# Performance work log

Hardware: AMD Instinct MI355X
Metric: run time of the kernel (lower is better)

The kernel has to match this reference:

```python
import jax, jax.numpy as jnp
import numpy as np

N = 50000   # nodes
E = 800000  # edges (avg degree 16)
H = 3       # attention heads
D_IN, D_HID, D_OUT = 256, 64, 10


def setup_inputs() -> dict:
    key = jax.random.key(0)
    ks = jax.random.split(key, 8)
    x = jax.random.normal(ks[0], (N, D_IN), dtype=jnp.float32)
    edge_index = jax.random.randint(ks[1], (2, E), 0, N, dtype=jnp.int64)
    W1 = jax.random.normal(ks[2], (H, D_IN, D_HID), dtype=jnp.float32) / np.sqrt(D_IN)
    a_src1 = jax.random.normal(ks[3], (H, D_HID), dtype=jnp.float32) / np.sqrt(D_HID)
    a_dst1 = jax.random.normal(ks[4], (H, D_HID), dtype=jnp.float32) / np.sqrt(D_HID)
    W2 = jax.random.normal(ks[5], (H, D_HID, D_OUT), dtype=jnp.float32) / np.sqrt(D_HID)
    a_src2 = jax.random.normal(ks[6], (H, D_OUT), dtype=jnp.float32) / np.sqrt(D_OUT)
    a_dst2 = jax.random.normal(ks[7], (H, D_OUT), dtype=jnp.float32) / np.sqrt(D_OUT)
    return {"x": x, "edge_index": edge_index, "W1": W1, "a_src1": a_src1,
            "a_dst1": a_dst1, "W2": W2, "a_src2": a_src2, "a_dst2": a_dst2}


def gat_layer(x, src, dst, W, a_s, a_d, n):
    # x: [N, Din]; W: [H, Din, Dout]; returns [N, Dout] (heads averaged)
    z = jnp.einsum('nd,hde->nhe', x, W)                     # [N, H, Dout]
    e_src = jnp.einsum('nhe,he->nh', z, a_s)[src]           # [E, H]
    e_dst = jnp.einsum('nhe,he->nh', z, a_d)[dst]           # [E, H]
    e = jax.nn.leaky_relu(e_src + e_dst, 0.2)               # [E, H]
    # numerically-stable softmax over incoming edges of each dst node
    m = jax.lax.stop_gradient(jax.ops.segment_max(e, dst, num_segments=n))
    ex = jnp.exp(e - m[dst])                                # [E, H]
    denom = jax.ops.segment_sum(ex, dst, num_segments=n)    # [N, H]
    alpha = ex / (denom[dst] + 1e-16)                       # [E, H]
    out = jax.ops.segment_sum(z[src] * alpha[:, :, None], dst, num_segments=n)
    return out.mean(axis=1)                                 # [N, Dout]


def reference(x, edge_index, W1, a_src1, a_dst1, W2, a_src2, a_dst2):
    n = x.shape[0]
    src, dst = edge_index[0], edge_index[1]
    # dropout layers are identity in eval/deterministic mode
    h = gat_layer(x, src, dst, W1, a_src1, a_dst1, n)
    h = jax.nn.elu(h)
    h = gat_layer(h, src, dst, W2, a_src2, a_dst2, n)
    return h, jax.nn.log_softmax(h, axis=1)
```

## Files before the change

### kernel.cpp

```cpp
#include <hip/hip_runtime.h>
#include <math.h>

#define DIN  256
#define DHID 64
#define NH   3
#define DOUT 10
#define CAP  64

typedef __attribute__((ext_vector_type(8))) short bf16x8;
typedef __attribute__((ext_vector_type(4))) float f32x4;

__device__ inline unsigned short f2bf(float f) {
    unsigned u = __builtin_bit_cast(unsigned, f);
    unsigned r = (u + 0x7FFFu + ((u >> 16) & 1u)) >> 16;
    return (unsigned short)r;
}
__device__ inline float bf2f(unsigned short s) {
    unsigned u = ((unsigned)s) << 16;
    return __builtin_bit_cast(float, u);
}
__device__ inline f32x4 cvt4(ushort4 z) {
    f32x4 r;
    r[0] = bf2f(z.x); r[1] = bf2f(z.y); r[2] = bf2f(z.z); r[3] = bf2f(z.w);
    return r;
}


__global__ __launch_bounds__(256) void repack_zero_kernel(const float* __restrict__ W1,
                                                          unsigned short* __restrict__ W1p,
                                                          int* __restrict__ cursor, int N) {
    int bid = blockIdx.x;
    int tid = threadIdx.x;
    if (bid < 192) {
        int idx = bid * 256 + tid;
        int j = idx & 7, l = (idx >> 3) & 63, q = (idx >> 9) & 7, t = idx >> 12;
        int c = t * 16 + (l & 15);
        int k = q * 32 + (l >> 4) * 8 + j;
        int h = c >> 6, jj = c & 63;
        W1p[idx] = f2bf(W1[h * 16384 + k * 64 + jj]);
    } else {
        int i = (bid - 192) * 256 + tid;
        if (i < N) cursor[i] = 0;
    }
}


__global__ __launch_bounds__(256) void scatter_kernel(const int* __restrict__ src,
                                                      const int* __restrict__ dst,
                                                      int* __restrict__ cursor,
                                                      unsigned short* __restrict__ esrcp, int E) {
    int i = blockIdx.x * 256 + threadIdx.x;
    if (i < E) {
        int d = dst[i];
        int s = src[i];
        int pos = atomicAdd(cursor + d, 1);
        if (pos < CAP) esrcp[d * CAP + pos] = (unsigned short)s;
    }
}


__global__ __launch_bounds__(128) void gemm1_mfma_kernel(const float* __restrict__ x,
                                                         const bf16x8* __restrict__ W1p,
                                                         const float* __restrict__ a_s,
                                                         const float* __restrict__ a_d,
                                                         unsigned short* __restrict__ z1bf,
                                                         float* __restrict__ s1,
                                                         float* __restrict__ d1, int n) {
    __shared__ unsigned short Xs[32][272];
    int tid = threadIdx.x;
    int w = tid >> 6, lane = tid & 63;
    int m = lane & 15, quad = lane >> 4;
    int n0 = blockIdx.x * 32;

    for (int i = tid; i < 2048; i += 128) {
        int r = i >> 6, c4 = i & 63;
        int nn = n0 + r;
        float4 a = (nn < n) ? *(const float4*)(x + (size_t)nn * 256 + c4 * 4)
                            : (float4){0.f, 0.f, 0.f, 0.f};
        ushort4 b;
        b.x = f2bf(a.x); b.y = f2bf(a.y); b.z = f2bf(a.z); b.w = f2bf(a.w);
        *(ushort4*)(&Xs[r][c4 * 4]) = b;
    }
    __syncthreads();

    int rloc = w * 16 + m;
    f32x4 acc[12];
    #pragma unroll
    for (int t = 0; t < 12; ++t) acc[t] = (f32x4){0.f, 0.f, 0.f, 0.f};
    #pragma unroll
    for (int q = 0; q < 8; ++q) {
        bf16x8 af = *(const bf16x8*)(&Xs[rloc][q * 32 + quad * 8]);
        #pragma unroll
        for (int t = 0; t < 12; ++t) {
            bf16x8 bfr = W1p[(t * 8 + q) * 64 + lane];
            acc[t] = __builtin_amdgcn_mfma_f32_16x16x32_bf16(af, bfr, acc[t], 0, 0, 0);
        }
    }
    __syncthreads();

    float as_r[12], ad_r[12];
    #pragma unroll
    for (int t = 0; t < 12; ++t) { as_r[t] = a_s[t * 16 + m]; ad_r[t] = a_d[t * 16 + m]; }

    #pragma unroll
    for (int reg = 0; reg < 4; ++reg) {
        int row_loc = w * 16 + quad * 4 + reg;
        int row_out = n0 + row_loc;
        bool ok = row_out < n;
        float ps[3] = {0.f, 0.f, 0.f}, pd[3] = {0.f, 0.f, 0.f};
        #pragma unroll
        for (int t = 0; t < 12; ++t) {
            float v = acc[t][reg];
            Xs[row_loc][t * 16 + m] = f2bf(v);
            ps[t >> 2] += v * as_r[t];
            pd[t >> 2] += v * ad_r[t];
        }
        #pragma unroll
        for (int h = 0; h < 3; ++h) {
            float s = ps[h], d = pd[h];
            #pragma unroll
            for (int msk = 1; msk < 16; msk <<= 1) {
                s += __shfl_xor(s, msk, 16);
                d += __shfl_xor(d, msk, 16);
            }
            if (ok && m == 0) { s1[row_out * 4 + h] = s; d1[row_out * 4 + h] = d; }
        }
    }
    __syncthreads();

    for (int i = tid; i < 1536; i += 128) {
        int r = i / 48, c4 = i % 48;
        int nn = n0 + r;
        if (nn < n)
            *(ushort4*)(z1bf + (size_t)nn * 192 + c4 * 4) = *(const ushort4*)(&Xs[r][c4 * 4]);
    }
}


__global__ __launch_bounds__(256) void agg1_gemm2_kernel(
        const int* __restrict__ cnts, const unsigned short* __restrict__ esrcp,
        const float* __restrict__ s1, const float* __restrict__ d1,
        const unsigned short* __restrict__ z1bf,
        const float* __restrict__ W2, const float* __restrict__ as2,
        const float* __restrict__ ad2,
        unsigned short* __restrict__ z2bf,
        float* __restrict__ s2, float* __restrict__ d2, int n) {
    __shared__ float Ws[64][32];
    __shared__ float wlds[4][196];
    __shared__ float hb[4][64];
    __shared__ float tb[4][64];
    int tid = threadIdx.x;
    int lane = tid & 63, wave = tid >> 6;

    for (int idx = tid; idx < 2048; idx += 256) {
        int kk = idx >> 5, c = idx & 31;
        float wv = 0.f;
        if (c < 30) {
            int h = c / 10, j = c % 10;
            wv = W2[(h * 64 + kk) * 10 + j];
        }
        Ws[kk][c] = wv;
    }
    __syncthreads();

    int v = blockIdx.x * 4 + wave;
    if (v >= n) return;
    int cnt = cnts[v]; if (cnt > CAP) cnt = CAP;
    int m16 = lane & 15;
    int grp = lane >> 4;
    int head = grp > 2 ? 2 : grp;
    bool rowact = lane < 48;
    float dv0 = d1[v * 4], dv1 = d1[v * 4 + 1], dv2 = d1[v * 4 + 2];
    float* wl = wlds[wave];

    int u_l = 0; float w0 = 0.f, w1 = 0.f, w2 = 0.f;
    if (lane < cnt) {
        u_l = (int)esrcp[v * CAP + lane];
        float4 sv = *(const float4*)(s1 + (size_t)u_l * 4);
        float e0 = sv.x + dv0; e0 = e0 > 0.f ? e0 : 0.2f * e0;
        float e1 = sv.y + dv1; e1 = e1 > 0.f ? e1 : 0.2f * e1;
        float e2 = sv.z + dv2; e2 = e2 > 0.f ? e2 : 0.2f * e2;
        w0 = __expf(e0); w1 = __expf(e1); w2 = __expf(e2);
    }
    wl[lane] = w0; wl[65 + lane] = w1; wl[130 + lane] = w2;
    float4 wv4 = *(const float4*)(&wl[head * 65 + m16 * 4]);
    float denp = wv4.x + wv4.y + wv4.z + wv4.w;
    #pragma unroll
    for (int msk = 1; msk < 16; msk <<= 1) denp += __shfl_xor(denp, msk, 16);

    f32x4 acc = (f32x4){0.f, 0.f, 0.f, 0.f};
    if (rowact) {
        int rnd = (cnt + 3) & ~3;
        const int wb = head * 65;
        for (int j = 0; j < rnd; j += 4) {
            int u0 = __builtin_amdgcn_readlane(u_l, j);
            int u1 = __builtin_amdgcn_readlane(u_l, j + 1);
            int u2 = __builtin_amdgcn_readlane(u_l, j + 2);
            int u3 = __builtin_amdgcn_readlane(u_l, j + 3);
            float wa = wl[wb + j], wb2 = wl[wb + j + 1];
            float wc = wl[wb + j + 2], wd = wl[wb + j + 3];
            ushort4 za = *(const ushort4*)(z1bf + (size_t)u0 * 192 + lane * 4);
            ushort4 zb = *(const ushort4*)(z1bf + (size_t)u1 * 192 + lane * 4);
            ushort4 zc = *(const ushort4*)(z1bf + (size_t)u2 * 192 + lane * 4);
            ushort4 zd = *(const ushort4*)(z1bf + (size_t)u3 * 192 + lane * 4);
            acc += cvt4(za) * wa;
            acc += cvt4(zb) * wb2;
            acc += cvt4(zc) * wc;
            acc += cvt4(zd) * wd;
        }
    }
    float invd = (1.f / 3.f) / (denp + 1e-16f);
    float acc0 = rowact ? acc[0] * invd : 0.f;
    float acc1 = rowact ? acc[1] * invd : 0.f;
    float acc2 = rowact ? acc[2] * invd : 0.f;
    float acc3 = rowact ? acc[3] * invd : 0.f;
    acc0 += __shfl_down(acc0, 32, 64); acc0 += __shfl_down(acc0, 16, 64);
    acc1 += __shfl_down(acc1, 32, 64); acc1 += __shfl_down(acc1, 16, 64);
    acc2 += __shfl_down(acc2, 32, 64); acc2 += __shfl_down(acc2, 16, 64);
    acc3 += __shfl_down(acc3, 32, 64); acc3 += __shfl_down(acc3, 16, 64);
    if (lane < 16) {
        float4 o;
        o.x = acc0 > 0.f ? acc0 : __expf(acc0) - 1.f;
        o.y = acc1 > 0.f ? acc1 : __expf(acc1) - 1.f;
        o.z = acc2 > 0.f ? acc2 : __expf(acc2) - 1.f;
        o.w = acc3 > 0.f ? acc3 : __expf(acc3) - 1.f;
        *(float4*)(&hb[wave][lane * 4]) = o;
    }

    int c = lane & 31, half = lane >> 5;
    float zc = 0.f;
    {
        int k0 = half * 32;
        #pragma unroll 8
        for (int k = 0; k < 32; ++k)
            zc += hb[wave][k0 + k] * Ws[k0 + k][c];
    }
    zc += __shfl_down(zc, 32, 64);
    if (lane < 32) {
        z2bf[(size_t)v * 32 + c] = f2bf(zc);
        if (c < 30) {
            tb[wave][c]      = zc * as2[c];
            tb[wave][32 + c] = zc * ad2[c];
        }
    }
    if (lane < 6) {
        int h = lane >> 1;
        int base = (lane & 1) * 32 + h * 10;
        float sum = 0.f;
        #pragma unroll
        for (int j = 0; j < 10; ++j) sum += tb[wave][base + j];
        if ((lane & 1) == 0) s2[v * 4 + h] = sum;
        else                 d2[v * 4 + h] = sum;
    }
}


__global__ __launch_bounds__(256) void agg2_kernel(const int* __restrict__ cnts,
                                                   const unsigned short* __restrict__ esrcp,
                                                   const float* __restrict__ s2,
                                                   const float* __restrict__ d2,
                                                   const unsigned short* __restrict__ z2bf,
                                                   float* __restrict__ out, int n) {
    __shared__ float wlds[4][196];
    __shared__ float dlds[4][4];
    int tid = threadIdx.x;
    int lane = tid & 63, wave = tid >> 6;
    int v = blockIdx.x * 4 + wave;
    if (v >= n) return;
    int cnt = cnts[v]; if (cnt > CAP) cnt = CAP;
    int c2 = lane & 15;
    int quad = lane >> 4;
    int headc = c2 < 5 ? 0 : (c2 < 10 ? 1 : 2);
    int headg = quad > 2 ? 2 : quad;
    float dv0 = d2[v * 4], dv1 = d2[v * 4 + 1], dv2 = d2[v * 4 + 2];
    float* wl = wlds[wave];

    int u_l = 0; float w0 = 0.f, w1 = 0.f, w2 = 0.f;
    if (lane < cnt) {
        u_l = (int)esrcp[v * CAP + lane];
        float4 sv = *(const float4*)(s2 + (size_t)u_l * 4);
        float e0 = sv.x + dv0; e0 = e0 > 0.f ? e0 : 0.2f * e0;
        float e1 = sv.y + dv1; e1 = e1 > 0.f ? e1 : 0.2f * e1;
        float e2 = sv.z + dv2; e2 = e2 > 0.f ? e2 : 0.2f * e2;
        w0 = __expf(e0); w1 = __expf(e1); w2 = __expf(e2);
    }
    wl[lane] = w0; wl[65 + lane] = w1; wl[130 + lane] = w2;
    float4 wv = *(const float4*)(&wl[headg * 65 + c2 * 4]);
    float denp = wv.x + wv.y + wv.z + wv.w;
    #pragma unroll
    for (int msk = 1; msk < 16; msk <<= 1) denp += __shfl_xor(denp, msk, 16);
    if (c2 == 0 && quad < 3) dlds[wave][quad] = denp;

    float ax = 0.f, ay = 0.f;
    int rnd = (cnt + 3) & ~3;
    const int wb = headc * 65;
    for (int j = 0; j < rnd; j += 4) {
        int u = __shfl(u_l, j + quad, 64);
        float w = wl[wb + j + quad];
        ushort2 z = *(const ushort2*)(z2bf + (size_t)u * 32 + c2 * 2);
        ax += w * bf2f(z.x);
        ay += w * bf2f(z.y);
    }
    float den = dlds[wave][headc];
    ax += __shfl_down(ax, 32, 64); ax += __shfl_down(ax, 16, 64);
    ay += __shfl_down(ay, 32, 64); ay += __shfl_down(ay, 16, 64);
    float inv = 1.f / (den + 1e-16f);
    float rx = ax * inv, ry = ay * inv;
    float rx5  = __shfl(rx, lane + 5, 64);
    float rx10 = __shfl(rx, lane + 10, 64);
    float ry5  = __shfl(ry, lane + 5, 64);
    float ry10 = __shfl(ry, lane + 10, 64);
    float rrx = (rx + rx5 + rx10) * (1.f / 3.f);
    float rry = (ry + ry5 + ry10) * (1.f / 3.f);
    bool act = lane < 5;
    float mx = act ? fmaxf(rrx, rry) : -1e30f;
    #pragma unroll
    for (int msk = 1; msk < 8; msk <<= 1) mx = fmaxf(mx, __shfl_xor(mx, msk, 8));
    float e = act ? (__expf(rrx - mx) + __expf(rry - mx)) : 0.f;
    #pragma unroll
    for (int msk = 1; msk < 8; msk <<= 1) e += __shfl_xor(e, msk, 8);
    float lg = __logf(e);
    if (act) {
        float2 o1; o1.x = rrx; o1.y = rry;
        float2 o2; o2.x = rrx - mx - lg; o2.y = rry - mx - lg;
        *(float2*)(out + (size_t)v * DOUT + c2 * 2) = o1;
        *(float2*)(out + (size_t)n * DOUT + (size_t)v * DOUT + c2 * 2) = o2;
    }
}


extern "C" void kernel_launch(void* const* d_in, const int* in_sizes, int n_in,
                              void* d_out, int out_size, void* d_ws, size_t ws_size,
                              hipStream_t stream) {
    const float* x   = (const float*)d_in[0];
    const int*   ei  = (const int*)d_in[1];
    const float* W1  = (const float*)d_in[2];
    const float* as1 = (const float*)d_in[3];
    const float* ad1 = (const float*)d_in[4];
    const float* W2  = (const float*)d_in[5];
    const float* as2 = (const float*)d_in[6];
    const float* ad2 = (const float*)d_in[7];
    float* out = (float*)d_out;

    const int N = in_sizes[0] / DIN;
    const int E = in_sizes[1] / 2;
    const int* src = ei;
    const int* dst = ei + E;

    char* p = (char*)d_ws;
    auto alloc = [&](size_t bytes) -> void* {
        void* r = (void*)p;
        p += (bytes + 255) & ~(size_t)255;
        return r;
    };
    int* cursor  = (int*)alloc((size_t)N * 4);
    unsigned short* esrcp = (unsigned short*)alloc((size_t)N * CAP * 2);
    unsigned short* W1p  = (unsigned short*)alloc((size_t)49152 * 2);
    unsigned short* z1bf = (unsigned short*)alloc((size_t)N * 192 * 2);
    float* s1    = (float*)alloc((size_t)N * 4 * 4);
    float* d1    = (float*)alloc((size_t)N * 4 * 4);
    unsigned short* z2bf = (unsigned short*)alloc((size_t)N * 32 * 2);
    float* s2    = (float*)alloc((size_t)N * 4 * 4);
    float* d2    = (float*)alloc((size_t)N * 4 * 4);
    (void)alloc(512);

    repack_zero_kernel<<<192 + (N + 255) / 256, 256, 0, stream>>>(W1, W1p, cursor, N);
    scatter_kernel<<<(E + 255) / 256, 256, 0, stream>>>(src, dst, cursor, esrcp, E);

    gemm1_mfma_kernel<<<(N + 31) / 32, 128, 0, stream>>>(x, (const bf16x8*)W1p, as1, ad1,
                                                         z1bf, s1, d1, N);
    agg1_gemm2_kernel<<<(N + 3) / 4, 256, 0, stream>>>(cursor, esrcp, s1, d1, z1bf,
                                                       W2, as2, ad2, z2bf, s2, d2, N);
    agg2_kernel<<<(N + 3) / 4, 256, 0, stream>>>(cursor, esrcp, s2, d2, z2bf, out, N);
}
```

Before: 262.4 us.

## Fuse edge scatter into GEMM1 launch, prerepack W2, software-pipeline aggregation gathers

Edge bucketing now runs as extra blocks inside the layer-1 GEMM launch, so the atomic scatter overlaps the MFMA work and one launch goes away. W2 is repacked once in the setup kernel into a padded layout, so each aggregation block copies it with vector loads instead of redoing the index arithmetic. Both neighbour aggregation loops now prefetch the next batch of gathered rows before accumulating the current one, to hide gather latency, and the small layer-2 GEMM uses two accumulators. The cost is more registers in the aggregation kernels and wasted work on padded neighbour slots, since the count is rounded up to 8.

```diff
diff --git a/kernel.cpp b/kernel.cpp
--- a/kernel.cpp
+++ b/kernel.cpp
@@ -27,10 +27,13 @@
 
 
 __global__ __launch_bounds__(256) void repack_zero_kernel(const float* __restrict__ W1,
+                                                          const float* __restrict__ W2,
                                                           unsigned short* __restrict__ W1p,
+                                                          float* __restrict__ W2cat,
                                                           int* __restrict__ cursor, int N) {
     int bid = blockIdx.x;
     int tid = threadIdx.x;
+    int nzb = (N + 255) >> 8;
     if (bid < 192) {
         int idx = bid * 256 + tid;
         int j = idx & 7, l = (idx >> 3) & 63, q = (idx >> 9) & 7, t = idx >> 12;
@@ -38,35 +41,48 @@
         int k = q * 32 + (l >> 4) * 8 + j;
         int h = c >> 6, jj = c & 63;
         W1p[idx] = f2bf(W1[h * 16384 + k * 64 + jj]);
-    } else {
+    } else if (bid < 192 + nzb) {
         int i = (bid - 192) * 256 + tid;
         if (i < N) cursor[i] = 0;
-    }
-}
-
-
-__global__ __launch_bounds__(256) void scatter_kernel(const int* __restrict__ src,
-                                                      const int* __restrict__ dst,
-                                                      int* __restrict__ cursor,
-                                                      unsigned short* __restrict__ esrcp, int E) {
-    int i = blockIdx.x * 256 + threadIdx.x;
-    if (i < E) {
-        int d = dst[i];
-        int s = src[i];
-        int pos = atomicAdd(cursor + d, 1);
-        if (pos < CAP) esrcp[d * CAP + pos] = (unsigned short)s;
-    }
-}
-
-
-__global__ __launch_bounds__(128) void gemm1_mfma_kernel(const float* __restrict__ x,
-                                                         const bf16x8* __restrict__ W1p,
-                                                         const float* __restrict__ a_s,
-                                                         const float* __restrict__ a_d,
-                                                         unsigned short* __restrict__ z1bf,
-                                                         float* __restrict__ s1,
-                                                         float* __restrict__ d1, int n) {
+    } else {
+        int idx = (bid - 192 - nzb) * 256 + tid;
+        if (idx < 2048) {
+            int kk = idx >> 5, c = idx & 31;
+            float wv = 0.f;
+            if (c < 30) {
+                int h = c / 10, j = c % 10;
+                wv = W2[(h * 64 + kk) * 10 + j];
+            }
+            W2cat[idx] = wv;
+        }
+    }
+}
+
+
+__global__ __launch_bounds__(128) void gemm1_scatter_kernel(const float* __restrict__ x,
+                                                            const bf16x8* __restrict__ W1p,
+                                                            const float* __restrict__ a_s,
+                                                            const float* __restrict__ a_d,
+                                                            unsigned short* __restrict__ z1bf,
+                                                            float* __restrict__ s1,
+                                                            float* __restrict__ d1, int n,
+                                                            const int* __restrict__ src,
+                                                            const int* __restrict__ dst,
+                                                            int* __restrict__ cursor,
+                                                            unsigned short* __restrict__ esrcp,
+                                                            int E, int G) {
     __shared__ unsigned short Xs[32][272];
+    if ((int)blockIdx.x >= G) {
+        int i = (blockIdx.x - G) * 128 + threadIdx.x;
+        if (i < E) {
+            int d = dst[i];
+            int s = src[i];
+            int pos = atomicAdd(cursor + d, 1);
+            if (pos < CAP) esrcp[d * CAP + pos] = (unsigned short)s;
+        }
+        return;
+    }
+
     int tid = threadIdx.x;
     int w = tid >> 6, lane = tid & 63;
     int m = lane & 15, quad = lane >> 4;
@@ -141,7 +157,7 @@
         const int* __restrict__ cnts, const unsigned short* __restrict__ esrcp,
         const float* __restrict__ s1, const float* __restrict__ d1,
         const unsigned short* __restrict__ z1bf,
-        const float* __restrict__ W2, const float* __restrict__ as2,
+        const float* __restrict__ W2cat, const float* __restrict__ as2,
         const float* __restrict__ ad2,
         unsigned short* __restrict__ z2bf,
         float* __restrict__ s2, float* __restrict__ d2, int n) {
@@ -152,15 +168,8 @@
     int tid = threadIdx.x;
     int lane = tid & 63, wave = tid >> 6;
 
-    for (int idx = tid; idx < 2048; idx += 256) {
-        int kk = idx >> 5, c = idx & 31;
-        float wv = 0.f;
-        if (c < 30) {
-            int h = c / 10, j = c % 10;
-            wv = W2[(h * 64 + kk) * 10 + j];
-        }
-        Ws[kk][c] = wv;
-    }
+    for (int idx = tid; idx < 1024; idx += 256)
+        ((float2*)&Ws[0][0])[idx] = ((const float2*)W2cat)[idx];
     __syncthreads();
 
     int v = blockIdx.x * 4 + wave;
@@ -183,32 +192,40 @@
         w0 = __expf(e0); w1 = __expf(e1); w2 = __expf(e2);
     }
     wl[lane] = w0; wl[65 + lane] = w1; wl[130 + lane] = w2;
+
+    f32x4 acc = (f32x4){0.f, 0.f, 0.f, 0.f};
+    if (rowact) {
+        int rnd = (cnt + 7) & ~7;
+        const int wb = head * 65;
+        ushort4 zr[8]; float wr[8];
+        #pragma unroll
+        for (int i = 0; i < 8; ++i) {
+            int u = __builtin_amdgcn_readlane(u_l, i);
+            zr[i] = *(const ushort4*)(z1bf + (size_t)u * 192 + lane * 4);
+            wr[i] = wl[wb + i];
+        }
+        for (int j = 8; j < rnd; j += 8) {
+            ushort4 zn[8]; float wn[8];
+            #pragma unroll
+            for (int i = 0; i < 8; ++i) {
+                int u = __builtin_amdgcn_readlane(u_l, j + i);
+                zn[i] = *(const ushort4*)(z1bf + (size_t)u * 192 + lane * 4);
+                wn[i] = wl[wb + j + i];
+            }
+            #pragma unroll
+            for (int i = 0; i < 8; ++i) acc += cvt4(zr[i]) * wr[i];
+            #pragma unroll
+            for (int i = 0; i < 8; ++i) { zr[i] = zn[i]; wr[i] = wn[i]; }
+        }
+        #pragma unroll
+        for (int i = 0; i < 8; ++i) acc += cvt4(zr[i]) * wr[i];
+    }
+
     float4 wv4 = *(const float4*)(&wl[head * 65 + m16 * 4]);
     float denp = wv4.x + wv4.y + wv4.z + wv4.w;
     #pragma unroll
     for (int msk = 1; msk < 16; msk <<= 1) denp += __shfl_xor(denp, msk, 16);
 
-    f32x4 acc = (f32x4){0.f, 0.f, 0.f, 0.f};
-    if (rowact) {
-        int rnd = (cnt + 3) & ~3;
-        const int wb = head * 65;
-        for (int j = 0; j < rnd; j += 4) {
-            int u0 = __builtin_amdgcn_readlane(u_l, j);
-            int u1 = __builtin_amdgcn_readlane(u_l, j + 1);
-            int u2 = __builtin_amdgcn_readlane(u_l, j + 2);
-            int u3 = __builtin_amdgcn_readlane(u_l, j + 3);
-            float wa = wl[wb + j], wb2 = wl[wb + j + 1];
-            float wc = wl[wb + j + 2], wd = wl[wb + j + 3];
-            ushort4 za = *(const ushort4*)(z1bf + (size_t)u0 * 192 + lane * 4);
-            ushort4 zb = *(const ushort4*)(z1bf + (size_t)u1 * 192 + lane * 4);
-            ushort4 zc = *(const ushort4*)(z1bf + (size_t)u2 * 192 + lane * 4);
-            ushort4 zd = *(const ushort4*)(z1bf + (size_t)u3 * 192 + lane * 4);
-            acc += cvt4(za) * wa;
-            acc += cvt4(zb) * wb2;
-            acc += cvt4(zc) * wc;
-            acc += cvt4(zd) * wd;
-        }
-    }
     float invd = (1.f / 3.f) / (denp + 1e-16f);
     float acc0 = rowact ? acc[0] * invd : 0.f;
     float acc1 = rowact ? acc[1] * invd : 0.f;
@@ -228,13 +245,14 @@
     }
 
     int c = lane & 31, half = lane >> 5;
-    float zc = 0.f;
-    {
-        int k0 = half * 32;
-        #pragma unroll 8
-        for (int k = 0; k < 32; ++k)
-            zc += hb[wave][k0 + k] * Ws[k0 + k][c];
-    }
+    int k0 = half * 32;
+    float zc0 = 0.f, zc1 = 0.f;
+    #pragma unroll
+    for (int k = 0; k < 32; k += 2) {
+        zc0 += hb[wave][k0 + k]     * Ws[k0 + k][c];
+        zc1 += hb[wave][k0 + k + 1] * Ws[k0 + k + 1][c];
+    }
+    float zc = zc0 + zc1;
     zc += __shfl_down(zc, 32, 64);
     if (lane < 32) {
         z2bf[(size_t)v * 32 + c] = f2bf(zc);
@@ -285,23 +303,37 @@
         w0 = __expf(e0); w1 = __expf(e1); w2 = __expf(e2);
     }
     wl[lane] = w0; wl[65 + lane] = w1; wl[130 + lane] = w2;
+
+    float ax = 0.f, ay = 0.f;
+    {
+        int rnd = (cnt + 7) & ~7;
+        const int wb = headc * 65;
+        int ua = __shfl(u_l, quad, 64);
+        int ub = __shfl(u_l, 4 + quad, 64);
+        float wa = wl[wb + quad], wbb = wl[wb + 4 + quad];
+        ushort2 za = *(const ushort2*)(z2bf + (size_t)ua * 32 + c2 * 2);
+        ushort2 zb = *(const ushort2*)(z2bf + (size_t)ub * 32 + c2 * 2);
+        for (int j = 8; j < rnd; j += 8) {
+            int un1 = __shfl(u_l, j + quad, 64);
+            int un2 = __shfl(u_l, j + 4 + quad, 64);
+            float wn1 = wl[wb + j + quad], wn2 = wl[wb + j + 4 + quad];
+            ushort2 zn1 = *(const ushort2*)(z2bf + (size_t)un1 * 32 + c2 * 2);
+            ushort2 zn2 = *(const ushort2*)(z2bf + (size_t)un2 * 32 + c2 * 2);
+            ax += wa * bf2f(za.x) + wbb * bf2f(zb.x);
+            ay += wa * bf2f(za.y) + wbb * bf2f(zb.y);
+            wa = wn1; wbb = wn2; za = zn1; zb = zn2;
+        }
+        ax += wa * bf2f(za.x) + wbb * bf2f(zb.x);
+        ay += wa * bf2f(za.y) + wbb * bf2f(zb.y);
+    }
+
     float4 wv = *(const float4*)(&wl[headg * 65 + c2 * 4]);
     float denp = wv.x + wv.y + wv.z + wv.w;
     #pragma unroll
     for (int msk = 1; msk < 16; msk <<= 1) denp += __shfl_xor(denp, msk, 16);
     if (c2 == 0 && quad < 3) dlds[wave][quad] = denp;
-
-    float ax = 0.f, ay = 0.f;
-    int rnd = (cnt + 3) & ~3;
-    const int wb = headc * 65;
-    for (int j = 0; j < rnd; j += 4) {
-        int u = __shfl(u_l, j + quad, 64);
-        float w = wl[wb + j + quad];
-        ushort2 z = *(const ushort2*)(z2bf + (size_t)u * 32 + c2 * 2);
-        ax += w * bf2f(z.x);
-        ay += w * bf2f(z.y);
-    }
     float den = dlds[wave][headc];
+
     ax += __shfl_down(ax, 32, 64); ax += __shfl_down(ax, 16, 64);
     ay += __shfl_down(ay, 32, 64); ay += __shfl_down(ay, 16, 64);
     float inv = 1.f / (den + 1e-16f);
@@ -356,6 +388,7 @@
     int* cursor  = (int*)alloc((size_t)N * 4);
     unsigned short* esrcp = (unsigned short*)alloc((size_t)N * CAP * 2);
     unsigned short* W1p  = (unsigned short*)alloc((size_t)49152 * 2);
+    float* W2cat = (float*)alloc((size_t)2048 * 4);
     unsigned short* z1bf = (unsigned short*)alloc((size_t)N * 192 * 2);
     float* s1    = (float*)alloc((size_t)N * 4 * 4);
     float* d1    = (float*)alloc((size_t)N * 4 * 4);
@@ -364,12 +397,16 @@
     float* d2    = (float*)alloc((size_t)N * 4 * 4);
     (void)alloc(512);
 
-    repack_zero_kernel<<<192 + (N + 255) / 256, 256, 0, stream>>>(W1, W1p, cursor, N);
-    scatter_kernel<<<(E + 255) / 256, 256, 0, stream>>>(src, dst, cursor, esrcp, E);
-
-    gemm1_mfma_kernel<<<(N + 31) / 32, 128, 0, stream>>>(x, (const bf16x8*)W1p, as1, ad1,
-                                                         z1bf, s1, d1, N);
+    int nzb = (N + 255) / 256;
+    repack_zero_kernel<<<192 + nzb + 8, 256, 0, stream>>>(W1, W2, W1p, W2cat, cursor, N);
+
+    int G = (N + 31) / 32;
+    int S = (E + 127) / 128;
+    gemm1_scatter_kernel<<<G + S, 128, 0, stream>>>(x, (const bf16x8*)W1p, as1, ad1,
+                                                    z1bf, s1, d1, N,
+                                                    src, dst, cursor, esrcp, E, G);
+
     agg1_gemm2_kernel<<<(N + 3) / 4, 256, 0, stream>>>(cursor, esrcp, s1, d1, z1bf,
-                                                       W2, as2, ad2, z2bf, s2, d2, N);
+                                                       W2cat, as2, ad2, z2bf, s2, d2, N);
     agg2_kernel<<<(N + 3) / 4, 256, 0, stream>>>(cursor, esrcp, s2, d2, z2bf, out, N);
 }
```

Result: no change. 262.5 us (+0.0%).
